# Performance work log

Hardware: AMD Instinct MI355X
Metric: run time of the kernel (lower is better)

The kernel has to match this reference:

```python
import jax, jax.numpy as jnp
import numpy as np

B, S, F, D = 8, 2048, 32, 256
EPS = 1e-5


def layer_norm(x, g, b):
    mu = jnp.mean(x, axis=-1, keepdims=True)
    var = jnp.mean(jnp.square(x - mu), axis=-1, keepdims=True)
    return (x - mu) * jax.lax.rsqrt(var + EPS) * g + b


def setup_inputs() -> dict:
    key = jax.random.key(0)
    ks = jax.random.split(key, 6)
    x = jax.random.normal(ks[0], (B, S, F), dtype=jnp.float32)
    # per-feature Linear(1, d): weight [F, D], bias [F, D]
    W = jax.random.normal(ks[1], (F, D), dtype=jnp.float32) * 0.1
    b = jax.random.normal(ks[2], (F, D), dtype=jnp.float32) * 0.1
    # score head: shared LayerNorm(D) + Linear(D, 1)
    ln1_g = jnp.ones((D,), dtype=jnp.float32)
    ln1_b = jnp.zeros((D,), dtype=jnp.float32)
    score_w = jax.random.normal(ks[3], (D,), dtype=jnp.float32) * 0.1
    score_b = jax.random.normal(ks[4], (), dtype=jnp.float32) * 0.1
    out_g = jnp.ones((D,), dtype=jnp.float32)
    out_b = jnp.zeros((D,), dtype=jnp.float32)
    return {"x": x, "W": W, "b": b, "ln1_g": ln1_g, "ln1_b": ln1_b,
            "score_w": score_w, "score_b": score_b, "out_g": out_g, "out_b": out_b}


def reference(x, W, b, ln1_g, ln1_b, score_w, score_b, out_g, out_b):
    # z[b,s,f,d] = x[b,s,f] * W[f,d] + b[f,d]  (per-feature Linear(1, D))
    z = x[..., None] * W + b                      # [B,S,F,D]
    h = jax.nn.gelu(layer_norm(z, ln1_g, ln1_b), approximate=False)
    scores = jnp.einsum('bsfd,d->bsf', h, score_w) + score_b  # [B,S,F]
    weights = jax.nn.softmax(scores, axis=-1)
    selected = jnp.einsum('bsfd,bsf->bsd', z, weights)        # [B,S,D]
    out = layer_norm(selected, out_g, out_b)
    return out, weights
```

## Files before the change

### kernel.cpp

```cpp
#include <hip/hip_runtime.h>
#include <math.h>

#define NB 8
#define NS 2048
#define NF 32
#define ND 256
#define NTOK (NB * NS)

#define TBL_N 2048

#if __has_builtin(__builtin_amdgcn_exp2f)
#define EXP2(x) __builtin_amdgcn_exp2f(x)
#else
#define EXP2(x) exp2f(x)
#endif

template <int CTRL, int RM>
__device__ __forceinline__ float dpp_step(float v) {
    int t = __builtin_amdgcn_update_dpp(0, __float_as_int(v), CTRL, RM, 0xf, true);
    return v + __int_as_float(t);
}
__device__ __forceinline__ float wave_sum63(float v) {
    v = dpp_step<0x111, 0xf>(v);
    v = dpp_step<0x112, 0xf>(v);
    v = dpp_step<0x114, 0xf>(v);
    v = dpp_step<0x118, 0xf>(v);
    v = dpp_step<0x142, 0xa>(v);
    v = dpp_step<0x143, 0xc>(v);
    return v;
}
__device__ __forceinline__ float lane63(float v) {
    return __int_as_float(__builtin_amdgcn_readlane(__float_as_int(v), 63));
}
__device__ __forceinline__ float rl(float v, int lane) {
    return __int_as_float(__builtin_amdgcn_readlane(__float_as_int(v), lane));
}

__global__ void vsn_stats(const float* __restrict__ W, const float* __restrict__ bias,
                          float* __restrict__ stats) {
    const int f = blockIdx.x;
    const int lane = threadIdx.x;
    const float4 w4 = *(const float4*)(W + f * ND + (lane << 2));
    const float4 b4 = *(const float4*)(bias + f * ND + (lane << 2));
    float sw  = (w4.x + w4.y) + (w4.z + w4.w);
    float sb  = (b4.x + b4.y) + (b4.z + b4.w);
    float sww = fmaf(w4.x, w4.x, fmaf(w4.y, w4.y, fmaf(w4.z, w4.z, w4.w * w4.w)));
    float swb = fmaf(w4.x, b4.x, fmaf(w4.y, b4.y, fmaf(w4.z, b4.z, w4.w * b4.w)));
    float sbb = fmaf(b4.x, b4.x, fmaf(b4.y, b4.y, fmaf(b4.z, b4.z, b4.w * b4.w)));
#pragma unroll
    for (int m = 32; m >= 1; m >>= 1) {
        sw += __shfl_xor(sw, m);  sb += __shfl_xor(sb, m);
        sww += __shfl_xor(sww, m); swb += __shfl_xor(swb, m); sbb += __shfl_xor(sbb, m);
    }
    if (lane == 0) {
        const float inv_d = 1.0f / ND;
        stats[f]        = sw * inv_d;
        stats[32 + f]   = sb * inv_d;
        stats[64 + f]   = sww * inv_d;
        stats[96 + f]   = swb * inv_d;
        stats[128 + f]  = sbb * inv_d;
    }
}

__global__ void vsn_table(float2* __restrict__ tbl) {
    const int i = blockIdx.x * 256 + threadIdx.x;
    if (i < TBL_N) {
        const float x0 = ((float)i - 1024.0f) * 0.015625f;
        const float x1 = x0 + 0.015625f;
        const float g0 = 0.5f * x0 * (1.0f + erff(x0 * 0.70710678118654752f));
        const float g1 = 0.5f * x1 * (1.0f + erff(x1 * 0.70710678118654752f));
        const float sb = (g1 - g0) * 0.125f;
        const float a  = g0 - (float)(8 * i) * sb;
        tbl[i] = make_float2(a, sb);
    }
}

__global__ __launch_bounds__(256, 4) void vsn_kernel(
    const float* __restrict__ x,
    const float* __restrict__ W,
    const float* __restrict__ bias,
    const float* __restrict__ stats,
    const float2* __restrict__ gtbl,
    const float* __restrict__ ln1g,
    const float* __restrict__ ln1b,
    const float* __restrict__ scw,
    const float* __restrict__ scb,
    const float* __restrict__ outg,
    const float* __restrict__ outb,
    float* __restrict__ out,
    float* __restrict__ wout)
{
    __shared__ float2 tab[TBL_N];
    for (int i = threadIdx.x; i < TBL_N; i += 256) tab[i] = gtbl[i];
    __syncthreads();

    const int lane = threadIdx.x & 63;
    const int wid  = threadIdx.x >> 6;
    const int tok  = (blockIdx.x << 2) | wid;
    const int d0   = lane << 2;
    const int fl   = lane & 31;

    constexpr float inv_d = 1.0f / 256.0f;
    constexpr float LOG2E = 1.4426950408889634f;
    const float TBL_MAX = 16383.0f;

    const float xv = x[tok * NF + fl];

    const float mu_l  = fmaf(xv, stats[fl], stats[32 + fl]);
    const float ez2   = fmaf(xv * xv, stats[64 + fl],
                             fmaf(xv + xv, stats[96 + fl], stats[128 + fl]));
    const float var_l = fmaf(-mu_l, mu_l, ez2);
    const float rs_l  = rsqrtf(var_l + 1e-5f);
    const float t2_l  = -mu_l * rs_l;

    const float4 g4f  = *(const float4*)(ln1g + d0);
    const float4 b4f  = *(const float4*)(ln1b + d0);
    const float4 sw4f = *(const float4*)(scw + d0);

    const float ga = g4f.x * 512.0f, gb = g4f.y * 512.0f;
    const float gc = g4f.z * 512.0f, gd = g4f.w * 512.0f;
    const float oa = fmaf(b4f.x, 512.0f, 8192.0f), ob = fmaf(b4f.y, 512.0f, 8192.0f);
    const float oc = fmaf(b4f.z, 512.0f, 8192.0f), od = fmaf(b4f.w, 512.0f, 8192.0f);
    const float q0 = sw4f.x * LOG2E, q1 = sw4f.y * LOG2E;
    const float q2 = sw4f.z * LOG2E, q3 = sw4f.w * LOG2E;
    const float Kv = scb[0] * LOG2E * 0.015625f;

    float s0 = 0.f, s1 = 0.f, s2 = 0.f, s3 = 0.f;
    float epark = 0.f;

#pragma unroll 4
    for (int f = 0; f < NF; ++f) {
        const float xf  = rl(xv, f);
        const float rsf = rl(rs_l, f);
        const float t2f = rl(t2_l, f);

        const float4 w4 = *(const float4*)(W + f * ND + d0);
        const float4 c4 = *(const float4*)(bias + f * ND + d0);

        const float z0 = fmaf(xf, w4.x, c4.x);
        const float z1 = fmaf(xf, w4.y, c4.y);
        const float z2 = fmaf(xf, w4.z, c4.z);
        const float z3 = fmaf(xf, w4.w, c4.w);

        const float t0 = fmaf(z0, rsf, t2f);
        const float t1 = fmaf(z1, rsf, t2f);
        const float t2 = fmaf(z2, rsf, t2f);
        const float t3 = fmaf(z3, rsf, t2f);

        const float u0 = fmaf(t0, ga, oa);
        const float u1 = fmaf(t1, gb, ob);
        const float u2 = fmaf(t2, gc, oc);
        const float u3 = fmaf(t3, gd, od);

        const float uc0 = __builtin_amdgcn_fmed3f(u0, 0.0f, TBL_MAX);
        const float uc1 = __builtin_amdgcn_fmed3f(u1, 0.0f, TBL_MAX);
        const float uc2 = __builtin_amdgcn_fmed3f(u2, 0.0f, TBL_MAX);
        const float uc3 = __builtin_amdgcn_fmed3f(u3, 0.0f, TBL_MAX);

        const int i0 = ((int)uc0) & ~7;
        const int i1 = ((int)uc1) & ~7;
        const int i2 = ((int)uc2) & ~7;
        const int i3 = ((int)uc3) & ~7;

        const float2 T0 = *(const float2*)((const char*)tab + i0);
        const float2 T1 = *(const float2*)((const char*)tab + i1);
        const float2 T2 = *(const float2*)((const char*)tab + i2);
        const float2 T3 = *(const float2*)((const char*)tab + i3);

        const float h0 = fmaf(uc0, T0.y, T0.x);
        const float h1 = fmaf(uc1, T1.y, T1.x);
        const float h2 = fmaf(uc2, T2.y, T2.x);
        const float h3 = fmaf(uc3, T3.y, T3.x);

        const float dp = fmaf(h0, q0, fmaf(h1, q1, fmaf(h2, q2, fmaf(h3, q3, Kv))));

        const float e = EXP2(lane63(wave_sum63(dp)));

        epark = (lane == f) ? e : epark;
        s0 = fmaf(e, z0, s0);
        s1 = fmaf(e, z1, s1);
        s2 = fmaf(e, z2, s2);
        s3 = fmaf(e, z3, s3);
    }

    const float den = lane63(wave_sum63(epark));
    const float invden = __builtin_amdgcn_rcpf(den);

    const float v0 = s0 * invden, v1 = s1 * invden;
    const float v2 = s2 * invden, v3 = s3 * invden;

    const float su = lane63(wave_sum63((v0 + v1) + (v2 + v3)));
    const float qu = lane63(wave_sum63(
        fmaf(v0, v0, fmaf(v1, v1, fmaf(v2, v2, v3 * v3)))));
    const float mu  = su * inv_d;
    const float var = fmaf(-mu, mu, qu * inv_d);
    const float rso = rsqrtf(var + 1e-5f);

    const float4 og4 = *(const float4*)(outg + d0);
    const float4 ob4 = *(const float4*)(outb + d0);
    float4 o;
    o.x = fmaf((v0 - mu) * rso, og4.x, ob4.x);
    o.y = fmaf((v1 - mu) * rso, og4.y, ob4.y);
    o.z = fmaf((v2 - mu) * rso, og4.z, ob4.z);
    o.w = fmaf((v3 - mu) * rso, og4.w, ob4.w);
    *(float4*)(out + tok * ND + d0) = o;

    if (lane < NF) wout[tok * NF + lane] = epark * invden;
}

extern "C" void kernel_launch(void* const* d_in, const int* in_sizes, int n_in,
                              void* d_out, int out_size, void* d_ws, size_t ws_size,
                              hipStream_t stream) {
    const float* x    = (const float*)d_in[0];
    const float* W    = (const float*)d_in[1];
    const float* bias = (const float*)d_in[2];
    const float* ln1g = (const float*)d_in[3];
    const float* ln1b = (const float*)d_in[4];
    const float* scw  = (const float*)d_in[5];
    const float* scb  = (const float*)d_in[6];
    const float* outg = (const float*)d_in[7];
    const float* outb = (const float*)d_in[8];

    float*  stats = (float*)d_ws;
    float2* tbl   = (float2*)((char*)d_ws + 1024);
    float*  out   = (float*)d_out;
    float*  wout  = out + (size_t)NTOK * ND;

    hipLaunchKernelGGL(vsn_stats, dim3(NF), dim3(64), 0, stream, W, bias, stats);
    hipLaunchKernelGGL(vsn_table, dim3((TBL_N + 255) / 256), dim3(256), 0, stream, tbl);
    hipLaunchKernelGGL(vsn_kernel, dim3(NTOK / 4), dim3(256), 0, stream,
                       x, W, bias, stats, tbl, ln1g, ln1b, scw, scb, outg, outb, out, wout);
}
```

Measured before the change: 61.95 us.

## Process two tokens per wavefront with half-wave reductions and prefetched bpermute broadcasts

Each wavefront now handles two tokens, with 32 lanes per token and 8 D-elements per lane. The wave reduction is shortened to half-wave sums, and per-feature scalars are broadcast with ds_bpermute, prefetched one iteration ahead, instead of readlane. This halves the grid and amortizes the LDS table fill and per-token reduction overhead across more work. The cost is higher register pressure from 8-wide arrays and a doubled Kv split (0.03125) to match the 32-lane sum.

```diff
diff --git a/kernel.cpp b/kernel.cpp
--- a/kernel.cpp
+++ b/kernel.cpp
@@ -20,20 +20,19 @@
     int t = __builtin_amdgcn_update_dpp(0, __float_as_int(v), CTRL, RM, 0xf, true);
     return v + __int_as_float(t);
 }
-__device__ __forceinline__ float wave_sum63(float v) {
+__device__ __forceinline__ float wave_sum_halves(float v) {
     v = dpp_step<0x111, 0xf>(v);
     v = dpp_step<0x112, 0xf>(v);
     v = dpp_step<0x114, 0xf>(v);
     v = dpp_step<0x118, 0xf>(v);
     v = dpp_step<0x142, 0xa>(v);
-    v = dpp_step<0x143, 0xc>(v);
     return v;
-}
-__device__ __forceinline__ float lane63(float v) {
-    return __int_as_float(__builtin_amdgcn_readlane(__float_as_int(v), 63));
 }
 __device__ __forceinline__ float rl(float v, int lane) {
     return __int_as_float(__builtin_amdgcn_readlane(__float_as_int(v), lane));
+}
+__device__ __forceinline__ float bp(int byteidx, float v) {
+    return __int_as_float(__builtin_amdgcn_ds_bpermute(byteidx, __float_as_int(v)));
 }
 
 __global__ void vsn_stats(const float* __restrict__ W, const float* __restrict__ bias,
@@ -96,116 +95,138 @@
 
     const int lane = threadIdx.x & 63;
     const int wid  = threadIdx.x >> 6;
-    const int tok  = (blockIdx.x << 2) | wid;
-    const int d0   = lane << 2;
-    const int fl   = lane & 31;
+    const int hi32 = lane & 32;
+    const int dl   = lane & 31;
+    const int tok  = (((blockIdx.x << 2) | wid) << 1) | (lane >> 5);
+    const int d0   = dl << 3;
 
     constexpr float inv_d = 1.0f / 256.0f;
     constexpr float LOG2E = 1.4426950408889634f;
     const float TBL_MAX = 16383.0f;
 
-    const float xv = x[tok * NF + fl];
-
-    const float mu_l  = fmaf(xv, stats[fl], stats[32 + fl]);
-    const float ez2   = fmaf(xv * xv, stats[64 + fl],
-                             fmaf(xv + xv, stats[96 + fl], stats[128 + fl]));
+    const float xv = x[tok * NF + dl];
+
+    const float mu_l  = fmaf(xv, stats[dl], stats[32 + dl]);
+    const float ez2   = fmaf(xv * xv, stats[64 + dl],
+                             fmaf(xv + xv, stats[96 + dl], stats[128 + dl]));
     const float var_l = fmaf(-mu_l, mu_l, ez2);
     const float rs_l  = rsqrtf(var_l + 1e-5f);
     const float t2_l  = -mu_l * rs_l;
 
-    const float4 g4f  = *(const float4*)(ln1g + d0);
-    const float4 b4f  = *(const float4*)(ln1b + d0);
-    const float4 sw4f = *(const float4*)(scw + d0);
-
-    const float ga = g4f.x * 512.0f, gb = g4f.y * 512.0f;
-    const float gc = g4f.z * 512.0f, gd = g4f.w * 512.0f;
-    const float oa = fmaf(b4f.x, 512.0f, 8192.0f), ob = fmaf(b4f.y, 512.0f, 8192.0f);
-    const float oc = fmaf(b4f.z, 512.0f, 8192.0f), od = fmaf(b4f.w, 512.0f, 8192.0f);
-    const float q0 = sw4f.x * LOG2E, q1 = sw4f.y * LOG2E;
-    const float q2 = sw4f.z * LOG2E, q3 = sw4f.w * LOG2E;
-    const float Kv = scb[0] * LOG2E * 0.015625f;
-
-    float s0 = 0.f, s1 = 0.f, s2 = 0.f, s3 = 0.f;
+    float gg[8], oo[8], qq[8];
+    {
+        const float4 gA = *(const float4*)(ln1g + d0);
+        const float4 gB = *(const float4*)(ln1g + d0 + 4);
+        const float4 bA = *(const float4*)(ln1b + d0);
+        const float4 bB = *(const float4*)(ln1b + d0 + 4);
+        const float4 qA = *(const float4*)(scw + d0);
+        const float4 qB = *(const float4*)(scw + d0 + 4);
+        gg[0]=gA.x*512.f; gg[1]=gA.y*512.f; gg[2]=gA.z*512.f; gg[3]=gA.w*512.f;
+        gg[4]=gB.x*512.f; gg[5]=gB.y*512.f; gg[6]=gB.z*512.f; gg[7]=gB.w*512.f;
+        oo[0]=fmaf(bA.x,512.f,8192.f); oo[1]=fmaf(bA.y,512.f,8192.f);
+        oo[2]=fmaf(bA.z,512.f,8192.f); oo[3]=fmaf(bA.w,512.f,8192.f);
+        oo[4]=fmaf(bB.x,512.f,8192.f); oo[5]=fmaf(bB.y,512.f,8192.f);
+        oo[6]=fmaf(bB.z,512.f,8192.f); oo[7]=fmaf(bB.w,512.f,8192.f);
+        qq[0]=qA.x*LOG2E; qq[1]=qA.y*LOG2E; qq[2]=qA.z*LOG2E; qq[3]=qA.w*LOG2E;
+        qq[4]=qB.x*LOG2E; qq[5]=qB.y*LOG2E; qq[6]=qB.z*LOG2E; qq[7]=qB.w*LOG2E;
+    }
+    const float Kv = scb[0] * LOG2E * 0.03125f;
+
+    float ss[8];
+#pragma unroll
+    for (int k = 0; k < 8; ++k) ss[k] = 0.f;
     float epark = 0.f;
 
-#pragma unroll 4
+    float xf  = bp(hi32 << 2, xv);
+    float rsf = bp(hi32 << 2, rs_l);
+    float t2f = bp(hi32 << 2, t2_l);
+
+#pragma unroll 2
     for (int f = 0; f < NF; ++f) {
-        const float xf  = rl(xv, f);
-        const float rsf = rl(rs_l, f);
-        const float t2f = rl(t2_l, f);
-
-        const float4 w4 = *(const float4*)(W + f * ND + d0);
-        const float4 c4 = *(const float4*)(bias + f * ND + d0);
-
-        const float z0 = fmaf(xf, w4.x, c4.x);
-        const float z1 = fmaf(xf, w4.y, c4.y);
-        const float z2 = fmaf(xf, w4.z, c4.z);
-        const float z3 = fmaf(xf, w4.w, c4.w);
-
-        const float t0 = fmaf(z0, rsf, t2f);
-        const float t1 = fmaf(z1, rsf, t2f);
-        const float t2 = fmaf(z2, rsf, t2f);
-        const float t3 = fmaf(z3, rsf, t2f);
-
-        const float u0 = fmaf(t0, ga, oa);
-        const float u1 = fmaf(t1, gb, ob);
-        const float u2 = fmaf(t2, gc, oc);
-        const float u3 = fmaf(t3, gd, od);
-
-        const float uc0 = __builtin_amdgcn_fmed3f(u0, 0.0f, TBL_MAX);
-        const float uc1 = __builtin_amdgcn_fmed3f(u1, 0.0f, TBL_MAX);
-        const float uc2 = __builtin_amdgcn_fmed3f(u2, 0.0f, TBL_MAX);
-        const float uc3 = __builtin_amdgcn_fmed3f(u3, 0.0f, TBL_MAX);
-
-        const int i0 = ((int)uc0) & ~7;
-        const int i1 = ((int)uc1) & ~7;
-        const int i2 = ((int)uc2) & ~7;
-        const int i3 = ((int)uc3) & ~7;
-
-        const float2 T0 = *(const float2*)((const char*)tab + i0);
-        const float2 T1 = *(const float2*)((const char*)tab + i1);
-        const float2 T2 = *(const float2*)((const char*)tab + i2);
-        const float2 T3 = *(const float2*)((const char*)tab + i3);
-
-        const float h0 = fmaf(uc0, T0.y, T0.x);
-        const float h1 = fmaf(uc1, T1.y, T1.x);
-        const float h2 = fmaf(uc2, T2.y, T2.x);
-        const float h3 = fmaf(uc3, T3.y, T3.x);
-
-        const float dp = fmaf(h0, q0, fmaf(h1, q1, fmaf(h2, q2, fmaf(h3, q3, Kv))));
-
-        const float e = EXP2(lane63(wave_sum63(dp)));
-
-        epark = (lane == f) ? e : epark;
-        s0 = fmaf(e, z0, s0);
-        s1 = fmaf(e, z1, s1);
-        s2 = fmaf(e, z2, s2);
-        s3 = fmaf(e, z3, s3);
-    }
-
-    const float den = lane63(wave_sum63(epark));
+        const int bn = ((((f + 1) & 31)) | hi32) << 2;
+        const float xf_n  = bp(bn, xv);
+        const float rsf_n = bp(bn, rs_l);
+        const float t2f_n = bp(bn, t2_l);
+
+        const float4 wA = *(const float4*)(W + f * ND + d0);
+        const float4 wB = *(const float4*)(W + f * ND + d0 + 4);
+        const float4 cA = *(const float4*)(bias + f * ND + d0);
+        const float4 cB = *(const float4*)(bias + f * ND + d0 + 4);
+        const float wv[8] = {wA.x, wA.y, wA.z, wA.w, wB.x, wB.y, wB.z, wB.w};
+        const float cv[8] = {cA.x, cA.y, cA.z, cA.w, cB.x, cB.y, cB.z, cB.w};
+
+        float zz[8], hh[8];
+#pragma unroll
+        for (int k = 0; k < 8; ++k) {
+            const float z = fmaf(xf, wv[k], cv[k]);
+            zz[k] = z;
+            const float t = fmaf(z, rsf, t2f);
+            const float u = fmaf(t, gg[k], oo[k]);
+            const float uc = __builtin_amdgcn_fmed3f(u, 0.0f, TBL_MAX);
+            const int idx = ((int)uc) & ~7;
+            const float2 T = *(const float2*)((const char*)tab + idx);
+            hh[k] = fmaf(uc, T.y, T.x);
+        }
+
+        float dpA = fmaf(hh[0], qq[0], fmaf(hh[1], qq[1], fmaf(hh[2], qq[2], Kv)));
+        float dpB = fmaf(hh[3], qq[3], fmaf(hh[4], qq[4], hh[5] * qq[5]));
+        float dpC = fmaf(hh[6], qq[6], hh[7] * qq[7]);
+        const float dp = (dpA + dpB) + dpC;
+
+        const float ws = wave_sum_halves(dp);
+        const float sa = rl(ws, 31);
+        const float sb = rl(ws, 63);
+        const float e  = EXP2(hi32 ? sb : sa);
+
+        epark = (dl == f) ? e : epark;
+#pragma unroll
+        for (int k = 0; k < 8; ++k) ss[k] = fmaf(e, zz[k], ss[k]);
+
+        xf = xf_n; rsf = rsf_n; t2f = t2f_n;
+    }
+
+    const float wsd = wave_sum_halves(epark);
+    const float den = hi32 ? rl(wsd, 63) : rl(wsd, 31);
     const float invden = __builtin_amdgcn_rcpf(den);
 
-    const float v0 = s0 * invden, v1 = s1 * invden;
-    const float v2 = s2 * invden, v3 = s3 * invden;
-
-    const float su = lane63(wave_sum63((v0 + v1) + (v2 + v3)));
-    const float qu = lane63(wave_sum63(
-        fmaf(v0, v0, fmaf(v1, v1, fmaf(v2, v2, v3 * v3)))));
+    float vv[8];
+    float vsum = 0.f, vsq = 0.f;
+#pragma unroll
+    for (int k = 0; k < 8; ++k) {
+        vv[k] = ss[k] * invden;
+        vsum += vv[k];
+        vsq = fmaf(vv[k], vv[k], vsq);
+    }
+
+    const float wsu = wave_sum_halves(vsum);
+    const float su  = hi32 ? rl(wsu, 63) : rl(wsu, 31);
+    const float wsq = wave_sum_halves(vsq);
+    const float qu  = hi32 ? rl(wsq, 63) : rl(wsq, 31);
+
     const float mu  = su * inv_d;
     const float var = fmaf(-mu, mu, qu * inv_d);
     const float rso = rsqrtf(var + 1e-5f);
 
-    const float4 og4 = *(const float4*)(outg + d0);
-    const float4 ob4 = *(const float4*)(outb + d0);
-    float4 o;
-    o.x = fmaf((v0 - mu) * rso, og4.x, ob4.x);
-    o.y = fmaf((v1 - mu) * rso, og4.y, ob4.y);
-    o.z = fmaf((v2 - mu) * rso, og4.z, ob4.z);
-    o.w = fmaf((v3 - mu) * rso, og4.w, ob4.w);
-    *(float4*)(out + tok * ND + d0) = o;
-
-    if (lane < NF) wout[tok * NF + lane] = epark * invden;
+    const float4 ogA = *(const float4*)(outg + d0);
+    const float4 ogB = *(const float4*)(outg + d0 + 4);
+    const float4 obA = *(const float4*)(outb + d0);
+    const float4 obB = *(const float4*)(outb + d0 + 4);
+    const float og[8] = {ogA.x, ogA.y, ogA.z, ogA.w, ogB.x, ogB.y, ogB.z, ogB.w};
+    const float ob[8] = {obA.x, obA.y, obA.z, obA.w, obB.x, obB.y, obB.z, obB.w};
+
+    float4 oA, oB;
+    oA.x = fmaf((vv[0] - mu) * rso, og[0], ob[0]);
+    oA.y = fmaf((vv[1] - mu) * rso, og[1], ob[1]);
+    oA.z = fmaf((vv[2] - mu) * rso, og[2], ob[2]);
+    oA.w = fmaf((vv[3] - mu) * rso, og[3], ob[3]);
+    oB.x = fmaf((vv[4] - mu) * rso, og[4], ob[4]);
+    oB.y = fmaf((vv[5] - mu) * rso, og[5], ob[5]);
+    oB.z = fmaf((vv[6] - mu) * rso, og[6], ob[6]);
+    oB.w = fmaf((vv[7] - mu) * rso, og[7], ob[7]);
+    *(float4*)(out + tok * ND + d0) = oA;
+    *(float4*)(out + tok * ND + d0 + 4) = oB;
+
+    wout[tok * NF + dl] = epark * invden;
 }
 
 extern "C" void kernel_launch(void* const* d_in, const int* in_sizes, int n_in,
@@ -228,6 +249,6 @@
 
     hipLaunchKernelGGL(vsn_stats, dim3(NF), dim3(64), 0, stream, W, bias, stats);
     hipLaunchKernelGGL(vsn_table, dim3((TBL_N + 255) / 256), dim3(256), 0, stream, tbl);
-    hipLaunchKernelGGL(vsn_kernel, dim3(NTOK / 4), dim3(256), 0, stream,
+    hipLaunchKernelGGL(vsn_kernel, dim3(NTOK / 8), dim3(256), 0, stream,
                        x, W, bias, stats, tbl, ln1g, ln1b, scw, scb, outg, outb, out, wout);
 }
```

Result: faster. 59.00 us (-4.8%).
